# Performance work log

Measured on AMD Instinct MI355X. Metric: run time of the kernel, lower is better.

The kernel has to match this reference:

```python
import jax, jax.numpy as jnp
import numpy as np

N = 50000        # nodes
E = 800000       # edges (avg degree 16)
G = 512          # graphs in batch
H = 128          # hidden_channels
F = 128          # num_filters
NG = 50          # num_gaussians
NI = 6           # num_interactions
CUTOFF = 10.0


def ssp(x):
    # shifted softplus: softplus(x) - log(2)
    return jax.nn.softplus(x) - jnp.log(2.0).astype(x.dtype)


def setup_inputs() -> dict:
    key = jax.random.key(0)
    ks = jax.random.split(key, 16)
    z = jax.random.randint(ks[0], (N,), 0, 100)
    pos = jax.random.uniform(ks[1], (N, 3), jnp.float32) * 5.0  # box keeps d < cutoff
    batch = jnp.sort(jax.random.randint(ks[2], (N,), 0, G))
    row = jax.random.randint(ks[3], (E,), 0, N)
    off = jax.random.randint(ks[4], (E,), 1, N)
    col = (row + off) % N  # no self loops -> d > 0
    edge_index = jnp.stack([row, col])
    s = 0.1
    emb = jax.random.normal(ks[5], (100, H), jnp.float32) * s
    w1 = jax.random.normal(ks[6], (NI, NG, F), jnp.float32) * s
    b1 = jnp.zeros((NI, F), jnp.float32)
    w2 = jax.random.normal(ks[7], (NI, F, F), jnp.float32) * s
    b2 = jnp.zeros((NI, F), jnp.float32)
    lin1_w = jax.random.normal(ks[8], (NI, H, F), jnp.float32) * s   # no bias
    lin2_w = jax.random.normal(ks[9], (NI, F, H), jnp.float32) * s
    lin2_b = jnp.zeros((NI, H), jnp.float32)
    lin_w = jax.random.normal(ks[10], (NI, H, H), jnp.float32) * s
    lin_b = jnp.zeros((NI, H), jnp.float32)
    out_w1 = jax.random.normal(ks[11], (H, H // 2), jnp.float32) * s
    out_b1 = jnp.zeros((H // 2,), jnp.float32)
    out_w2 = jax.random.normal(ks[12], (H // 2, 1), jnp.float32) * s
    out_b2 = jnp.zeros((1,), jnp.float32)
    return dict(pos=pos, emb=emb, w1=w1, b1=b1, w2=w2, b2=b2,
                lin1_w=lin1_w, lin2_w=lin2_w, lin2_b=lin2_b,
                lin_w=lin_w, lin_b=lin_b,
                out_w1=out_w1, out_b1=out_b1, out_w2=out_w2, out_b2=out_b2,
                z=z, batch=batch, edge_index=edge_index)


def reference(pos, emb, w1, b1, w2, b2, lin1_w, lin2_w, lin2_b, lin_w, lin_b,
              out_w1, out_b1, out_w2, out_b2, z, batch, edge_index):
    row, col = edge_index[0], edge_index[1]  # row = target i, col = source j
    diff = pos[row] - pos[col]               # [E,3]
    d = jnp.sqrt(jnp.sum(diff * diff, axis=-1) + 1e-12)  # [E]

    # Gaussian smearing (PyG): exp(coeff * (d - offset)^2)
    offset = jnp.linspace(0.0, CUTOFF, NG, dtype=jnp.float32)
    coeff = -0.5 / (offset[1] - offset[0]) ** 2
    rbf = jnp.exp(coeff * (d[:, None] - offset) ** 2)  # [E,NG]

    # cosine cutoff
    C = 0.5 * (jnp.cos(d * (jnp.pi / CUTOFF)) + 1.0)    # [E]

    h = emb[z]  # [N,H]
    for i in range(NI):
        # filter network on edge RBF features
        W = ssp(rbf @ w1[i] + b1[i]) @ w2[i] + b2[i]    # [E,F]
        W = W * C[:, None]
        x = h @ lin1_w[i]                               # [N,F]
        msg = x[col] * W                                # gather + modulate [E,F]
        agg = jax.ops.segment_sum(msg, row, num_segments=N)  # scatter-add [N,F]
        x = agg @ lin2_w[i] + lin2_b[i]                 # [N,H]
        x = ssp(x)
        x = x @ lin_w[i] + lin_b[i]
        h = h + x                                       # residual

    h = ssp(h @ out_w1 + out_b1)                        # [N,H//2]
    per_atom = h @ out_w2 + out_b2                      # [N,1]
    energy = jax.ops.segment_sum(per_atom, batch, num_segments=G)  # [G,1]
    return energy
```

## Files before the change

kernel.cpp:

```cpp
#include <hip/hip_runtime.h>
#include <math.h>


constexpr int Nn  = 50000;
constexpr int Ee  = 800000;
constexpr int Gg  = 512;
constexpr int Hh  = 128;
constexpr int NGg = 50;
constexpr int NIi = 6;
constexpr int TS  = 4096;
constexpr int NB  = (Nn + 255) / 256;
constexpr float DMAXv = 8.6603f;

typedef short bf16x8 __attribute__((ext_vector_type(8)));
typedef float f32x4  __attribute__((ext_vector_type(4)));

__device__ __forceinline__ float ssp(float v) {
    return log1pf(__expf(-fabsf(v))) + fmaxf(v, 0.0f) - 0.69314718056f;
}
__device__ __forceinline__ unsigned short f2bf(float f) {
    unsigned int u = __float_as_uint(f);
    u += 0x7fffu + ((u >> 16) & 1u);
    return (unsigned short)(u >> 16);
}
__device__ __forceinline__ float bf2f(unsigned int h) {
    return __uint_as_float(h << 16);
}

__global__ void k_embed(const float* __restrict__ emb, const int* __restrict__ z,
                        float* __restrict__ h) {
    int tid = blockIdx.x * 256 + threadIdx.x;
    int n = tid >> 7, f = tid & 127;
    h[tid] = emb[z[n] * Hh + f];
}

__global__ void k_hist(const int* __restrict__ ei, int* __restrict__ counts) {
    int e = blockIdx.x * 256 + threadIdx.x;
    if (e >= Ee) return;
    atomicAdd(&counts[ei[e]], 1);
}

__global__ __launch_bounds__(256) void k_scanA(const int* __restrict__ counts,
                                               int* __restrict__ incl,
                                               int* __restrict__ bsum) {
    int t = blockIdx.x * 256 + threadIdx.x;
    int lane = threadIdx.x & 63, wv = threadIdx.x >> 6;
    int c = (t < Nn) ? counts[t] : 0;
    int v = c;
    #pragma unroll
    for (int off = 1; off < 64; off <<= 1) {
        int u = __shfl_up(v, off);
        if (lane >= off) v += u;
    }
    __shared__ int ws[4];
    if (lane == 63) ws[wv] = v;
    __syncthreads();
    if (threadIdx.x == 0) {
        int s = 0;
        #pragma unroll
        for (int i = 0; i < 4; ++i) { int x = ws[i]; ws[i] = s; s += x; }
        bsum[blockIdx.x] = s;
    }
    __syncthreads();
    v += ws[wv];
    if (t < Nn) incl[t] = v;
}

__global__ __launch_bounds__(256) void k_scanB(int* __restrict__ bsum) {
    __shared__ int s[256];
    int t = threadIdx.x;
    int v = (t < NB) ? bsum[t] : 0;
    s[t] = v;
    __syncthreads();
    for (int off = 1; off < 256; off <<= 1) {
        int u = (t >= off) ? s[t - off] : 0;
        __syncthreads();
        s[t] += u;
        __syncthreads();
    }
    if (t < NB) bsum[t] = s[t] - v;
}

__global__ __launch_bounds__(256) void k_scanC(const int* __restrict__ counts,
                                               const int* __restrict__ incl,
                                               const int* __restrict__ bsum,
                                               int* __restrict__ offsets,
                                               int* __restrict__ cursor) {
    int t = blockIdx.x * 256 + threadIdx.x;
    if (t >= Nn) return;
    int off = bsum[blockIdx.x] + incl[t] - counts[t];
    offsets[t] = off;
    cursor[t]  = off;
    if (t == Nn - 1) offsets[Nn] = off + counts[t];
}

__global__ void k_scatter(const int* __restrict__ ei, const float* __restrict__ pos,
                          int* __restrict__ cursor, int2* __restrict__ payload,
                          float inv_step) {
    int e = blockIdx.x * 256 + threadIdx.x;
    if (e >= Ee) return;
    int r = ei[e], c = ei[Ee + e];
    float dx = pos[3 * r    ] - pos[3 * c    ];
    float dy = pos[3 * r + 1] - pos[3 * c + 1];
    float dz = pos[3 * r + 2] - pos[3 * c + 2];
    float d = sqrtf(dx * dx + dy * dy + dz * dz + 1e-12f);
    float u = d * inv_step;
    if (u > (float)(TS - 1) - 5e-4f) u = (float)(TS - 1) - 5e-4f;
    int p = atomicAdd(&cursor[r], 1);
    payload[p] = make_int2(c, __float_as_int(u));
}

__global__ void k_pack(const float* __restrict__ lin1, const float* __restrict__ lin2,
                       const float* __restrict__ lin3, const float* __restrict__ ow1,
                       short* __restrict__ Wp) {
    int o = blockIdx.x * 256 + threadIdx.x;
    if (o < 18 * 16384) {
        int m = o >> 14, r = o & 16383;
        int k = (r >> 7) & 127, c = r & 127;
        int i = m / 3, which = m % 3;
        const float* src = which == 0 ? lin1 : (which == 1 ? lin2 : lin3);
        float v = src[(size_t)i * 16384 + k * 128 + c];
        int nt = c >> 4, lc = c & 15, kk = k >> 5, kg = (k >> 3) & 3, e = k & 7;
        int l = kg * 16 + lc;
        Wp[(size_t)m * 16384 + ((nt * 4 + kk) * 64 + l) * 8 + e] = (short)f2bf(v);
    } else {
        int r = o - 18 * 16384;
        int k = r >> 6, c = r & 63;
        float v = ow1[k * 64 + c];
        int nt = c >> 4, lc = c & 15, kk = k >> 5, kg = (k >> 3) & 3, e = k & 7;
        int l = kg * 16 + lc;
        Wp[(size_t)18 * 16384 + ((nt * 4 + kk) * 64 + l) * 8 + e] = (short)f2bf(v);
    }
}

__global__ __launch_bounds__(256) void k_table(
        const float* __restrict__ w1, const float* __restrict__ b1,
        const float* __restrict__ w2, const float* __restrict__ b2,
        unsigned short* __restrict__ T, float step) {
    __shared__ unsigned int w2p[64 * 128];
    __shared__ unsigned int w1p[25 * 128];
    __shared__ float rbf_s[2][NGg];
    __shared__ float tb[2][128];
    int tid = threadIdx.x;
    for (int i = tid; i < 64 * 128; i += 256) {
        int k2 = i >> 7, f = i & 127;
        unsigned int lo = f2bf(w2[(2 * k2) * 128 + f]);
        unsigned int hi = f2bf(w2[(2 * k2 + 1) * 128 + f]);
        w2p[i] = lo | (hi << 16);
    }
    for (int i = tid; i < 25 * 128; i += 256) {
        int k2 = i >> 7, f = i & 127;
        unsigned int lo = f2bf(w1[(2 * k2) * 128 + f]);
        unsigned int hi = f2bf(w1[(2 * k2 + 1) * 128 + f]);
        w1p[i] = lo | (hi << 16);
    }
    int jj = tid >> 7, f = tid & 127;
    float bb1 = b1[f], bb2 = b2[f];
    for (int p = 0; p < 4; ++p) {
        int j = blockIdx.x * 8 + p * 2 + jj;
        float dj = j * step;
        __syncthreads();
        if (f < NGg) {
            float u = dj - f * (10.0f / 49.0f);
            rbf_s[jj][f] = expf(-12.00500f * u * u);
        }
        __syncthreads();
        float u = bb1;
        for (int k2 = 0; k2 < 25; ++k2) {
            unsigned int wv = w1p[k2 * 128 + f];
            u = fmaf(rbf_s[jj][2 * k2    ], bf2f(wv & 0xffffu), u);
            u = fmaf(rbf_s[jj][2 * k2 + 1], bf2f(wv >> 16), u);
        }
        tb[jj][f] = ssp(u);
        __syncthreads();
        float w = bb2;
        for (int k2 = 0; k2 < 64; ++k2) {
            unsigned int wv = w2p[k2 * 128 + f];
            w = fmaf(tb[jj][2 * k2    ], bf2f(wv & 0xffffu), w);
            w = fmaf(tb[jj][2 * k2 + 1], bf2f(wv >> 16), w);
        }
        float C = 0.5f * (cosf(dj * 0.31415926535f) + 1.0f);
        T[j * 128 + f] = f2bf(w * C);
    }
}

__global__ __launch_bounds__(256) void k_mfma1(
        const float* __restrict__ in, const short* __restrict__ Wp,
        unsigned short* __restrict__ out, int nrows) {
    __shared__ short As[64 * 128];
    int tid = threadIdx.x;
    int base = blockIdx.x * 64;
    const float4* in4 = (const float4*)(in + (size_t)base * 128);
    int lim4 = (nrows - base) * 32;
    for (int i = tid; i < 2048; i += 256) {
        float4 v = make_float4(0.f, 0.f, 0.f, 0.f);
        if (i < lim4) v = in4[i];
        ushort4 o; o.x = f2bf(v.x); o.y = f2bf(v.y); o.z = f2bf(v.z); o.w = f2bf(v.w);
        int row = i >> 5, colg = i & 31;
        int byte = (row * 256 + colg * 8) ^ ((row & 7) << 4);
        *(ushort4*)((char*)As + byte) = o;
    }
    __syncthreads();

    int w = tid >> 6, lane = tid & 63;
    int arow = w * 16 + (lane & 15);
    bf16x8 a[4];
    #pragma unroll
    for (int kk = 0; kk < 4; ++kk) {
        int byte = (arow * 256 + kk * 64 + (lane >> 4) * 16) ^ ((arow & 7) << 4);
        a[kk] = *(const bf16x8*)((const char*)As + byte);
    }
    f32x4 acc[8];
    f32x4 zero = {0.f, 0.f, 0.f, 0.f};
    #pragma unroll
    for (int nt = 0; nt < 8; ++nt) acc[nt] = zero;
    const bf16x8* Wp8 = (const bf16x8*)Wp;
    #pragma unroll
    for (int nt = 0; nt < 8; ++nt)
        #pragma unroll
        for (int kk = 0; kk < 4; ++kk)
            acc[nt] = __builtin_amdgcn_mfma_f32_16x16x32_bf16(
                a[kk], Wp8[(nt * 4 + kk) * 64 + lane], acc[nt], 0, 0, 0);
    #pragma unroll
    for (int nt = 0; nt < 8; ++nt) {
        int col = nt * 16 + (lane & 15);
        #pragma unroll
        for (int r = 0; r < 4; ++r) {
            int row = base + w * 16 + (lane >> 4) * 4 + r;
            if (row < nrows) out[(size_t)row * 128 + col] = f2bf(acc[nt][r]);
        }
    }
}

__global__ __launch_bounds__(256) void k_fused(
        const float* __restrict__ agg, const short* __restrict__ W2p,
        const float* __restrict__ b2, const short* __restrict__ W3p,
        const float* __restrict__ b3, float* __restrict__ h,
        const short* __restrict__ Wnext, unsigned short* __restrict__ xb,
        const short* __restrict__ OW1p, const float* __restrict__ ob1,
        const float* __restrict__ ow2, const float* __restrict__ ob2,
        const int* __restrict__ batch, float* __restrict__ energy, int nrows) {
    __shared__ short As[64 * 128];
    __shared__ float rowsum[64];
    int tid = threadIdx.x;
    int base = blockIdx.x * 64;
    const float4* in4 = (const float4*)(agg + (size_t)base * 128);
    int lim4 = (nrows - base) * 32;
    for (int i = tid; i < 2048; i += 256) {
        float4 v = make_float4(0.f, 0.f, 0.f, 0.f);
        if (i < lim4) v = in4[i];
        ushort4 o; o.x = f2bf(v.x); o.y = f2bf(v.y); o.z = f2bf(v.z); o.w = f2bf(v.w);
        int row = i >> 5, colg = i & 31;
        int byte = (row * 256 + colg * 8) ^ ((row & 7) << 4);
        *(ushort4*)((char*)As + byte) = o;
    }
    __syncthreads();

    int w = tid >> 6, lane = tid & 63;
    int arow = w * 16 + (lane & 15);
    f32x4 zero = {0.f, 0.f, 0.f, 0.f};
    bf16x8 a[4];
    #pragma unroll
    for (int kk = 0; kk < 4; ++kk) {
        int byte = (arow * 256 + kk * 64 + (lane >> 4) * 16) ^ ((arow & 7) << 4);
        a[kk] = *(const bf16x8*)((const char*)As + byte);
    }
    f32x4 acc[8];
    #pragma unroll
    for (int nt = 0; nt < 8; ++nt) acc[nt] = zero;
    const bf16x8* W2p8 = (const bf16x8*)W2p;
    #pragma unroll
    for (int nt = 0; nt < 8; ++nt)
        #pragma unroll
        for (int kk = 0; kk < 4; ++kk)
            acc[nt] = __builtin_amdgcn_mfma_f32_16x16x32_bf16(
                a[kk], W2p8[(nt * 4 + kk) * 64 + lane], acc[nt], 0, 0, 0);

    #pragma unroll
    for (int nt = 0; nt < 8; ++nt) {
        int col = nt * 16 + (lane & 15);
        float bv = b2[col];
        #pragma unroll
        for (int r = 0; r < 4; ++r) {
            int row = w * 16 + (lane >> 4) * 4 + r;
            int byte = (row * 256 + col * 2) ^ ((row & 7) << 4);
            *(unsigned short*)((char*)As + byte) = f2bf(ssp(acc[nt][r] + bv));
        }
    }
    __syncthreads();

    bf16x8 a2[4];
    #pragma unroll
    for (int kk = 0; kk < 4; ++kk) {
        int byte = (arow * 256 + kk * 64 + (lane >> 4) * 16) ^ ((arow & 7) << 4);
        a2[kk] = *(const bf16x8*)((const char*)As + byte);
    }
    f32x4 acc2[8];
    #pragma unroll
    for (int nt = 0; nt < 8; ++nt) acc2[nt] = zero;
    const bf16x8* W3p8 = (const bf16x8*)W3p;
    #pragma unroll
    for (int nt = 0; nt < 8; ++nt)
        #pragma unroll
        for (int kk = 0; kk < 4; ++kk)
            acc2[nt] = __builtin_amdgcn_mfma_f32_16x16x32_bf16(
                a2[kk], W3p8[(nt * 4 + kk) * 64 + lane], acc2[nt], 0, 0, 0);

    bool last = (OW1p != nullptr);
    #pragma unroll
    for (int nt = 0; nt < 8; ++nt) {
        int col = nt * 16 + (lane & 15);
        float bv3 = b3[col];
        #pragma unroll
        for (int r = 0; r < 4; ++r) {
            int lrow = w * 16 + (lane >> 4) * 4 + r;
            int row = base + lrow;
            float hv = 0.f;
            if (row < nrows) hv = h[(size_t)row * 128 + col];
            float nv = hv + acc2[nt][r] + bv3;
            if (!last && row < nrows) h[(size_t)row * 128 + col] = nv;
            int byte = (lrow * 256 + col * 2) ^ ((lrow & 7) << 4);
            *(unsigned short*)((char*)As + byte) = f2bf(nv);
        }
    }
    __syncthreads();

    bf16x8 a3[4];
    #pragma unroll
    for (int kk = 0; kk < 4; ++kk) {
        int byte = (arow * 256 + kk * 64 + (lane >> 4) * 16) ^ ((arow & 7) << 4);
        a3[kk] = *(const bf16x8*)((const char*)As + byte);
    }

    if (!last) {
        f32x4 acc3[8];
        #pragma unroll
        for (int nt = 0; nt < 8; ++nt) acc3[nt] = zero;
        const bf16x8* Wn8 = (const bf16x8*)Wnext;
        #pragma unroll
        for (int nt = 0; nt < 8; ++nt)
            #pragma unroll
            for (int kk = 0; kk < 4; ++kk)
                acc3[nt] = __builtin_amdgcn_mfma_f32_16x16x32_bf16(
                    a3[kk], Wn8[(nt * 4 + kk) * 64 + lane], acc3[nt], 0, 0, 0);
        #pragma unroll
        for (int nt = 0; nt < 8; ++nt) {
            int col = nt * 16 + (lane & 15);
            #pragma unroll
            for (int r = 0; r < 4; ++r) {
                int row = base + w * 16 + (lane >> 4) * 4 + r;
                if (row < nrows) xb[(size_t)row * 128 + col] = f2bf(acc3[nt][r]);
            }
        }
    } else {
        f32x4 acc4[4];
        #pragma unroll
        for (int nt = 0; nt < 4; ++nt) acc4[nt] = zero;
        const bf16x8* W8 = (const bf16x8*)OW1p;
        #pragma unroll
        for (int nt = 0; nt < 4; ++nt)
            #pragma unroll
            for (int kk = 0; kk < 4; ++kk)
                acc4[nt] = __builtin_amdgcn_mfma_f32_16x16x32_bf16(
                    a3[kk], W8[(nt * 4 + kk) * 64 + lane], acc4[nt], 0, 0, 0);
        float p[4] = {0.f, 0.f, 0.f, 0.f};
        #pragma unroll
        for (int nt = 0; nt < 4; ++nt) {
            int col = nt * 16 + (lane & 15);
            float b = ob1[col], wv = ow2[col];
            #pragma unroll
            for (int r = 0; r < 4; ++r) p[r] += ssp(acc4[nt][r] + b) * wv;
        }
        #pragma unroll
        for (int m = 1; m < 16; m <<= 1) {
            #pragma unroll
            for (int r = 0; r < 4; ++r) p[r] += __shfl_xor(p[r], m);
        }
        if ((lane & 15) == 0) {
            #pragma unroll
            for (int r = 0; r < 4; ++r) rowsum[w * 16 + (lane >> 4) * 4 + r] = p[r];
        }
        __syncthreads();
        if (tid < 64) {
            int row = base + tid;
            int rc = row < nrows ? row : nrows - 1;
            int g = batch[rc];
            float v = (row < nrows) ? rowsum[tid] + ob2[0] : 0.f;
            #pragma unroll
            for (int off = 1; off < 64; off <<= 1) {
                float vo = __shfl_down(v, off);
                int   go = __shfl_down(g, off);
                if (tid + off < 64 && go == g) v += vo;
            }
            int gp = __shfl_up(g, 1);
            if (row < nrows && (tid == 0 || gp != g))
                unsafeAtomicAdd(&energy[g], v);
        }
    }
}

__device__ __forceinline__ void lerp_acc(unsigned int ta, unsigned int tb,
                                         unsigned int xv, float fr, float2& acc) {
    float t0a = bf2f(ta & 0xffffu), t0b = bf2f(ta >> 16);
    float t1a = bf2f(tb & 0xffffu), t1b = bf2f(tb >> 16);
    acc.x = fmaf(bf2f(xv & 0xffffu), fmaf(t1a - t0a, fr, t0a), acc.x);
    acc.y = fmaf(bf2f(xv >> 16),     fmaf(t1b - t0b, fr, t0b), acc.y);
}

__global__ __launch_bounds__(256) void k_agg(
        const int* __restrict__ offs, const int2* __restrict__ payload,
        const unsigned int* __restrict__ xw, const unsigned int* __restrict__ Tw,
        float* __restrict__ agg) {
    int wid = threadIdx.x >> 6, lane = threadIdx.x & 63;
    int n = blockIdx.x * 4 + wid;
    int beg = offs[n], end = offs[n + 1];
    float2 acc = make_float2(0.f, 0.f);
    int e = beg, cnt = end - beg;
    int2 p0, p1, p2, p3;
    if (cnt >= 4) { p0 = payload[e]; p1 = payload[e + 1]; p2 = payload[e + 2]; p3 = payload[e + 3]; }
    while (cnt >= 4) {
        unsigned int c0 = p0.x, c1 = p1.x, c2 = p2.x, c3 = p3.x;
        float u0 = __int_as_float(p0.y), u1 = __int_as_float(p1.y);
        float u2 = __int_as_float(p2.y), u3 = __int_as_float(p3.y);
        int j0 = (int)u0, j1 = (int)u1, j2 = (int)u2, j3 = (int)u3;
        float f0 = u0 - j0, f1 = u1 - j1, f2 = u2 - j2, f3 = u3 - j3;
        unsigned int ta0 = Tw[j0 * 64 + lane], tb0 = Tw[j0 * 64 + 64 + lane];
        unsigned int ta1 = Tw[j1 * 64 + lane], tb1 = Tw[j1 * 64 + 64 + lane];
        unsigned int ta2 = Tw[j2 * 64 + lane], tb2 = Tw[j2 * 64 + 64 + lane];
        unsigned int ta3 = Tw[j3 * 64 + lane], tb3 = Tw[j3 * 64 + 64 + lane];
        unsigned int xv0 = xw[(size_t)c0 * 64 + lane];
        unsigned int xv1 = xw[(size_t)c1 * 64 + lane];
        unsigned int xv2 = xw[(size_t)c2 * 64 + lane];
        unsigned int xv3 = xw[(size_t)c3 * 64 + lane];
        e += 4; cnt -= 4;
        if (cnt >= 4) { p0 = payload[e]; p1 = payload[e + 1]; p2 = payload[e + 2]; p3 = payload[e + 3]; }
        lerp_acc(ta0, tb0, xv0, f0, acc);
        lerp_acc(ta1, tb1, xv1, f1, acc);
        lerp_acc(ta2, tb2, xv2, f2, acc);
        lerp_acc(ta3, tb3, xv3, f3, acc);
    }
    for (; cnt > 0; --cnt, ++e) {
        int2 cur = payload[e];
        float u = __int_as_float(cur.y);
        int j = (int)u;
        float fr = u - (float)j;
        unsigned int ta = Tw[j * 64 + lane];
        unsigned int tb = Tw[j * 64 + 64 + lane];
        unsigned int xv = xw[(size_t)cur.x * 64 + lane];
        lerp_acc(ta, tb, xv, fr, acc);
    }
    ((float2*)agg)[(size_t)n * 64 + lane] = acc;
}

extern "C" void kernel_launch(void* const* d_in, const int* in_sizes, int n_in,
                              void* d_out, int out_size, void* d_ws, size_t ws_size,
                              hipStream_t stream) {
    const float* pos    = (const float*)d_in[0];
    const float* emb    = (const float*)d_in[1];
    const float* w1     = (const float*)d_in[2];
    const float* b1     = (const float*)d_in[3];
    const float* w2     = (const float*)d_in[4];
    const float* b2     = (const float*)d_in[5];
    const float* lin1_w = (const float*)d_in[6];
    const float* lin2_w = (const float*)d_in[7];
    const float* lin2_b = (const float*)d_in[8];
    const float* lin_w  = (const float*)d_in[9];
    const float* lin_b  = (const float*)d_in[10];
    const float* ow1    = (const float*)d_in[11];
    const float* ob1    = (const float*)d_in[12];
    const float* ow2    = (const float*)d_in[13];
    const float* ob2    = (const float*)d_in[14];
    const int*   z      = (const int*)d_in[15];
    const int*   batch  = (const int*)d_in[16];
    const int*   ei     = (const int*)d_in[17];
    float* energy = (float*)d_out;

    char* ws = (char*)d_ws;
    float*          h       = (float*)ws;          ws += (size_t)Nn * 128 * 4;
    float*          agg     = (float*)ws;          ws += (size_t)Nn * 128 * 4;
    unsigned short* xb      = (unsigned short*)ws; ws += (size_t)Nn * 128 * 2;
    unsigned short* T       = (unsigned short*)ws; ws += (size_t)TS * 128 * 2;
    int2*           payload = (int2*)ws;           ws += (size_t)Ee * 8;
    short*          Wp      = (short*)ws;          ws += ((size_t)18 * 16384 + 8192) * 2;
    int*            counts  = (int*)ws;            ws += (size_t)Nn * 4;
    int*            offsets = (int*)ws;            ws += (size_t)(Nn + 1) * 4;
    int*            cursor  = (int*)ws;            ws += (size_t)Nn * 4;
    int*            incl    = (int*)ws;            ws += (size_t)Nn * 4;
    int*            bsum    = (int*)ws;            ws += (size_t)256 * 4;

    float step = DMAXv / (TS - 1);
    float inv_step = (TS - 1) / DMAXv;

    hipMemsetAsync(d_out, 0, Gg * 4, stream);
    hipMemsetAsync(counts, 0, (size_t)Nn * 4, stream);
    k_embed<<<Nn * 128 / 256, 256, 0, stream>>>(emb, z, h);

    k_hist<<<(Ee + 255) / 256, 256, 0, stream>>>(ei, counts);
    k_scanA<<<NB, 256, 0, stream>>>(counts, incl, bsum);
    k_scanB<<<1, 256, 0, stream>>>(bsum);
    k_scanC<<<NB, 256, 0, stream>>>(counts, incl, bsum, offsets, cursor);
    k_scatter<<<(Ee + 255) / 256, 256, 0, stream>>>(ei, pos, cursor, payload, inv_step);

    k_pack<<<(18 * 16384 + 8192) / 256, 256, 0, stream>>>(lin1_w, lin2_w, lin_w, ow1, Wp);

    int gemm_blocks = (Nn + 63) / 64;
    const short* OWp = Wp + (size_t)18 * 16384;

    k_table<<<512, 256, 0, stream>>>(w1, b1, w2, b2, T, step);
    k_mfma1<<<gemm_blocks, 256, 0, stream>>>(h, Wp, xb, Nn);

    for (int i = 0; i < NIi; ++i) {
        const short* W2p = Wp + (size_t)(i * 3 + 1) * 16384;
        const short* W3p = Wp + (size_t)(i * 3 + 2) * 16384;
        bool last = (i == NIi - 1);
        const short* Wnext = last ? nullptr : Wp + (size_t)((i + 1) * 3) * 16384;

        k_agg<<<Nn / 4, 256, 0, stream>>>(offsets, payload,
                                          (const unsigned int*)xb, (const unsigned int*)T, agg);
        if (!last)
            k_table<<<512, 256, 0, stream>>>(w1 + (size_t)(i + 1) * NGg * 128,
                                             b1 + (size_t)(i + 1) * 128,
                                             w2 + (size_t)(i + 1) * 128 * 128,
                                             b2 + (size_t)(i + 1) * 128, T, step);
        k_fused<<<gemm_blocks, 256, 0, stream>>>(
            agg, W2p, lin2_b + (size_t)i * Hh, W3p, lin_b + (size_t)i * Hh, h,
            Wnext, xb, last ? OWp : nullptr, ob1, ow2, ob2, batch, energy, Nn);
    }
}
```

Before: 949.7 us.

## Store aggregation output as pre-swizzled bf16 and pair adjacent table rows

k_agg now packs its float accumulators to bf16 and writes them in the XOR-swizzled layout that k_fused uses in LDS. k_fused can then copy tiles straight into shared memory with no conversion, and the agg buffer moving through memory shrinks by half. A new k_pair kernel interleaves each filter-table row with the next one, so the interpolation in k_agg uses one 8-byte gather instead of two 4-byte gathers. This costs an extra small kernel per interaction and doubles the table footprint. Rounding the aggregate to bf16 before the GEMM adds a little precision loss.

```diff
diff --git a/kernel.cpp b/kernel.cpp
--- a/kernel.cpp
+++ b/kernel.cpp
@@ -184,6 +184,15 @@
     }
 }
 
+__global__ __launch_bounds__(256) void k_pair(const unsigned int* __restrict__ Tu,
+                                              uint2* __restrict__ Tp) {
+    int i = blockIdx.x * 256 + threadIdx.x;
+    int j = i >> 6, l = i & 63;
+    unsigned int a = Tu[j * 64 + l];
+    unsigned int b = (j < TS - 1) ? Tu[(j + 1) * 64 + l] : a;
+    Tp[i] = make_uint2(a, b);
+}
+
 __global__ __launch_bounds__(256) void k_mfma1(
         const float* __restrict__ in, const short* __restrict__ Wp,
         unsigned short* __restrict__ out, int nrows) {
@@ -233,7 +242,7 @@
 }
 
 __global__ __launch_bounds__(256) void k_fused(
-        const float* __restrict__ agg, const short* __restrict__ W2p,
+        const unsigned int* __restrict__ aggp, const short* __restrict__ W2p,
         const float* __restrict__ b2, const short* __restrict__ W3p,
         const float* __restrict__ b3, float* __restrict__ h,
         const short* __restrict__ Wnext, unsigned short* __restrict__ xb,
@@ -244,15 +253,11 @@
     __shared__ float rowsum[64];
     int tid = threadIdx.x;
     int base = blockIdx.x * 64;
-    const float4* in4 = (const float4*)(agg + (size_t)base * 128);
-    int lim4 = (nrows - base) * 32;
-    for (int i = tid; i < 2048; i += 256) {
-        float4 v = make_float4(0.f, 0.f, 0.f, 0.f);
-        if (i < lim4) v = in4[i];
-        ushort4 o; o.x = f2bf(v.x); o.y = f2bf(v.y); o.z = f2bf(v.z); o.w = f2bf(v.w);
-        int row = i >> 5, colg = i & 31;
-        int byte = (row * 256 + colg * 8) ^ ((row & 7) << 4);
-        *(ushort4*)((char*)As + byte) = o;
+    {
+        const uint4* gp = (const uint4*)aggp + (size_t)blockIdx.x * 1024;
+        uint4* As4 = (uint4*)As;
+        #pragma unroll
+        for (int i = 0; i < 4; ++i) As4[i * 256 + tid] = gp[i * 256 + tid];
     }
     __syncthreads();
 
@@ -409,8 +414,8 @@
 
 __global__ __launch_bounds__(256) void k_agg(
         const int* __restrict__ offs, const int2* __restrict__ payload,
-        const unsigned int* __restrict__ xw, const unsigned int* __restrict__ Tw,
-        float* __restrict__ agg) {
+        const unsigned int* __restrict__ xw, const uint2* __restrict__ Tp,
+        unsigned int* __restrict__ aggp) {
     int wid = threadIdx.x >> 6, lane = threadIdx.x & 63;
     int n = blockIdx.x * 4 + wid;
     int beg = offs[n], end = offs[n + 1];
@@ -424,32 +429,32 @@
         float u2 = __int_as_float(p2.y), u3 = __int_as_float(p3.y);
         int j0 = (int)u0, j1 = (int)u1, j2 = (int)u2, j3 = (int)u3;
         float f0 = u0 - j0, f1 = u1 - j1, f2 = u2 - j2, f3 = u3 - j3;
-        unsigned int ta0 = Tw[j0 * 64 + lane], tb0 = Tw[j0 * 64 + 64 + lane];
-        unsigned int ta1 = Tw[j1 * 64 + lane], tb1 = Tw[j1 * 64 + 64 + lane];
-        unsigned int ta2 = Tw[j2 * 64 + lane], tb2 = Tw[j2 * 64 + 64 + lane];
-        unsigned int ta3 = Tw[j3 * 64 + lane], tb3 = Tw[j3 * 64 + 64 + lane];
+        uint2 t0 = Tp[(size_t)j0 * 64 + lane];
+        uint2 t1 = Tp[(size_t)j1 * 64 + lane];
+        uint2 t2 = Tp[(size_t)j2 * 64 + lane];
+        uint2 t3 = Tp[(size_t)j3 * 64 + lane];
         unsigned int xv0 = xw[(size_t)c0 * 64 + lane];
         unsigned int xv1 = xw[(size_t)c1 * 64 + lane];
         unsigned int xv2 = xw[(size_t)c2 * 64 + lane];
         unsigned int xv3 = xw[(size_t)c3 * 64 + lane];
         e += 4; cnt -= 4;
         if (cnt >= 4) { p0 = payload[e]; p1 = payload[e + 1]; p2 = payload[e + 2]; p3 = payload[e + 3]; }
-        lerp_acc(ta0, tb0, xv0, f0, acc);
-        lerp_acc(ta1, tb1, xv1, f1, acc);
-        lerp_acc(ta2, tb2, xv2, f2, acc);
-        lerp_acc(ta3, tb3, xv3, f3, acc);
+        lerp_acc(t0.x, t0.y, xv0, f0, acc);
+        lerp_acc(t1.x, t1.y, xv1, f1, acc);
+        lerp_acc(t2.x, t2.y, xv2, f2, acc);
+        lerp_acc(t3.x, t3.y, xv3, f3, acc);
     }
     for (; cnt > 0; --cnt, ++e) {
         int2 cur = payload[e];
         float u = __int_as_float(cur.y);
         int j = (int)u;
         float fr = u - (float)j;
-        unsigned int ta = Tw[j * 64 + lane];
-        unsigned int tb = Tw[j * 64 + 64 + lane];
+        uint2 t = Tp[(size_t)j * 64 + lane];
         unsigned int xv = xw[(size_t)cur.x * 64 + lane];
-        lerp_acc(ta, tb, xv, fr, acc);
-    }
-    ((float2*)agg)[(size_t)n * 64 + lane] = acc;
+        lerp_acc(t.x, t.y, xv, fr, acc);
+    }
+    unsigned int ov = (unsigned int)f2bf(acc.x) | ((unsigned int)f2bf(acc.y) << 16);
+    aggp[(size_t)n * 64 + (((lane >> 2) ^ (n & 7)) << 2) + (lane & 3)] = ov;
 }
 
 extern "C" void kernel_launch(void* const* d_in, const int* in_sizes, int n_in,
@@ -477,9 +482,10 @@
 
     char* ws = (char*)d_ws;
     float*          h       = (float*)ws;          ws += (size_t)Nn * 128 * 4;
-    float*          agg     = (float*)ws;          ws += (size_t)Nn * 128 * 4;
+    unsigned int*   aggp    = (unsigned int*)ws;   ws += (size_t)Nn * 128 * 2;
     unsigned short* xb      = (unsigned short*)ws; ws += (size_t)Nn * 128 * 2;
     unsigned short* T       = (unsigned short*)ws; ws += (size_t)TS * 128 * 2;
+    uint2*          Tp      = (uint2*)ws;          ws += (size_t)TS * 64 * 8;
     int2*           payload = (int2*)ws;           ws += (size_t)Ee * 8;
     short*          Wp      = (short*)ws;          ws += ((size_t)18 * 16384 + 8192) * 2;
     int*            counts  = (int*)ws;            ws += (size_t)Nn * 4;
@@ -507,6 +513,7 @@
     const short* OWp = Wp + (size_t)18 * 16384;
 
     k_table<<<512, 256, 0, stream>>>(w1, b1, w2, b2, T, step);
+    k_pair<<<TS * 64 / 256, 256, 0, stream>>>((const unsigned int*)T, Tp);
     k_mfma1<<<gemm_blocks, 256, 0, stream>>>(h, Wp, xb, Nn);
 
     for (int i = 0; i < NIi; ++i) {
@@ -516,14 +523,16 @@
         const short* Wnext = last ? nullptr : Wp + (size_t)((i + 1) * 3) * 16384;
 
         k_agg<<<Nn / 4, 256, 0, stream>>>(offsets, payload,
-                                          (const unsigned int*)xb, (const unsigned int*)T, agg);
-        if (!last)
+                                          (const unsigned int*)xb, Tp, aggp);
+        if (!last) {
             k_table<<<512, 256, 0, stream>>>(w1 + (size_t)(i + 1) * NGg * 128,
                                              b1 + (size_t)(i + 1) * 128,
                                              w2 + (size_t)(i + 1) * 128 * 128,
                                              b2 + (size_t)(i + 1) * 128, T, step);
+            k_pair<<<TS * 64 / 256, 256, 0, stream>>>((const unsigned int*)T, Tp);
+        }
         k_fused<<<gemm_blocks, 256, 0, stream>>>(
-            agg, W2p, lin2_b + (size_t)i * Hh, W3p, lin_b + (size_t)i * Hh, h,
+            aggp, W2p, lin2_b + (size_t)i * Hh, W3p, lin_b + (size_t)i * Hh, h,
             Wnext, xb, last ? OWp : nullptr, ob1, ow2, ob2, batch, energy, Nn);
     }
 }
```

Result: slower. 974.5 us (+2.6%).
